# Kernel optimization log

Hardware: AMD Instinct MI355X
Metric: run time of the kernel (lower is better)

Reference implementation:

```python
import jax, jax.numpy as jnp
import numpy as np

N_NODES = 100000


def gcn_conv(x, edge_index, W, b):
    """PyG GCNConv: add self-loops, symmetric deg^-1/2 normalization, linear."""
    n = x.shape[0]
    h = x @ W  # [N, out]
    loop = jnp.arange(n, dtype=edge_index.dtype)
    src = jnp.concatenate([edge_index[0], loop])
    dst = jnp.concatenate([edge_index[1], loop])
    deg = jax.ops.segment_sum(jnp.ones_like(dst, dtype=h.dtype), dst, num_segments=n)
    dinv = jnp.where(deg > 0, jax.lax.rsqrt(deg), 0.0)
    norm = dinv[src] * dinv[dst]  # [E+N]
    msg = h[src] * norm[:, None]  # gather + scale
    out = jax.ops.segment_sum(msg, dst, num_segments=n)  # scatter-add
    return out + b


def setup_inputs() -> dict:
    key = jax.random.key(0)
    k1, k2, k3, k4 = jax.random.split(key, 4)
    d_in, d_hid, d_out = 128, 128, 128  # output_dim // 2 = 128
    E = 1600000
    x = jax.random.normal(k1, (N_NODES, d_in), dtype=jnp.float32)
    edge_index = jax.random.randint(k2, (2, E), 0, N_NODES, dtype=jnp.int64)
    s1 = 1.0 / np.sqrt(d_in)
    s2 = 1.0 / np.sqrt(d_hid)
    W1 = jax.random.normal(k3, (d_in, d_hid), dtype=jnp.float32) * s1
    b1 = jnp.zeros((d_hid,), dtype=jnp.float32)
    W2 = jax.random.normal(k4, (d_hid, d_out), dtype=jnp.float32) * s2
    b2 = jnp.zeros((d_out,), dtype=jnp.float32)
    return {"x": x, "edge_index": edge_index, "W1": W1, "b1": b1, "W2": W2, "b2": b2}


def reference(x, edge_index, W1, b1, W2, b2):
    h = jax.nn.relu(gcn_conv(x, edge_index, W1, b1))
    # dropout(p=0.5) is identity in eval mode
    return gcn_conv(h, edge_index, W2, b2)
```

## Files before the change

kernel.cpp:

```cpp
#include <hip/hip_runtime.h>

#define D 128

typedef unsigned int uint;
typedef unsigned short ushort;
typedef __attribute__((ext_vector_type(8))) short bf16x8_t;
typedef __attribute__((ext_vector_type(4))) float f32x4_t;

__global__ void k_init(int* __restrict__ degi, int n) {
    int i = blockIdx.x * blockDim.x + threadIdx.x;
    if (i < n) degi[i] = 1;
}

__global__ void k_count_rank(const int* __restrict__ dst, int* __restrict__ degi,
                             int* __restrict__ rank, int E) {
    int e = blockIdx.x * blockDim.x + threadIdx.x;
    if (e < E) rank[e] = atomicAdd(&degi[dst[e]], 1);
}

__global__ void k_dinv(const int* __restrict__ degi, float* __restrict__ dinv, int n) {
    int i = blockIdx.x * blockDim.x + threadIdx.x;
    if (i < n) dinv[i] = rsqrtf((float)degi[i]);
}

#define SCAN_BS 256
#define SCAN_ITEMS 4
#define SCAN_CHUNK (SCAN_BS * SCAN_ITEMS)

__device__ inline int count_at(const int* degi, int i, int n) {
    return (i < n) ? (degi[i] - 1) : 0;
}

__global__ void k_scan_partial(const int* __restrict__ degi, int* __restrict__ blockSums,
                               int n, int total) {
    __shared__ int s[SCAN_BS];
    int t = threadIdx.x;
    int base = blockIdx.x * SCAN_CHUNK + t * SCAN_ITEMS;
    int sum = 0;
    for (int j = 0; j < SCAN_ITEMS; j++) {
        int idx = base + j;
        if (idx < total) sum += count_at(degi, idx, n);
    }
    s[t] = sum; __syncthreads();
    for (int off = 1; off < SCAN_BS; off <<= 1) {
        int v = (t >= off) ? s[t - off] : 0;
        __syncthreads();
        s[t] += v;
        __syncthreads();
    }
    if (t == SCAN_BS - 1) blockSums[blockIdx.x] = s[t];
}

__global__ void k_scan_sums(int* __restrict__ blockSums, int nb) {
    __shared__ int s[1024];
    int t = threadIdx.x;
    int mine = (t < nb) ? blockSums[t] : 0;
    s[t] = mine; __syncthreads();
    for (int off = 1; off < 1024; off <<= 1) {
        int v = (t >= off) ? s[t - off] : 0;
        __syncthreads();
        s[t] += v;
        __syncthreads();
    }
    if (t < nb) blockSums[t] = s[t] - mine;
}

__global__ void k_scan_write(const int* __restrict__ degi, const int* __restrict__ blockSums,
                             int* __restrict__ row_ptr, int n, int total) {
    __shared__ int s[SCAN_BS];
    int t = threadIdx.x;
    int base = blockIdx.x * SCAN_CHUNK + t * SCAN_ITEMS;
    int c[SCAN_ITEMS];
    int sum = 0;
    for (int j = 0; j < SCAN_ITEMS; j++) {
        int idx = base + j;
        c[j] = (idx < total) ? count_at(degi, idx, n) : 0;
        sum += c[j];
    }
    int mine = sum;
    s[t] = sum; __syncthreads();
    for (int off = 1; off < SCAN_BS; off <<= 1) {
        int v = (t >= off) ? s[t - off] : 0;
        __syncthreads();
        s[t] += v;
        __syncthreads();
    }
    int off0 = blockSums[blockIdx.x] + (s[t] - mine);
    for (int j = 0; j < SCAN_ITEMS; j++) {
        int idx = base + j;
        if (idx < total) row_ptr[idx] = off0;
        off0 += c[j];
    }
}

__global__ void k_fill(const int* __restrict__ src, const int* __restrict__ dst,
                       const int* __restrict__ row_ptr, const int* __restrict__ rank,
                       int* __restrict__ col, int E) {
    int e = blockIdx.x * blockDim.x + threadIdx.x;
    if (e < E) {
        int d = dst[e];
        col[row_ptr[d] + rank[e] - 1] = src[e];
    }
}

__device__ inline uint bf16rn(float f) {
    uint u = __float_as_uint(f);
    return (u + 0x7fffu + ((u >> 16) & 1u)) >> 16;
}

__device__ inline void accum_bf16x8(float* a, uint4 v) {
    a[0] += __uint_as_float(v.x << 16);
    a[1] += __uint_as_float(v.x & 0xffff0000u);
    a[2] += __uint_as_float(v.y << 16);
    a[3] += __uint_as_float(v.y & 0xffff0000u);
    a[4] += __uint_as_float(v.z << 16);
    a[5] += __uint_as_float(v.z & 0xffff0000u);
    a[6] += __uint_as_float(v.w << 16);
    a[7] += __uint_as_float(v.w & 0xffff0000u);
}

__global__ void k_prep_w(const float* __restrict__ W, ushort* __restrict__ Wh,
                         ushort* __restrict__ Wl) {
    int i = blockIdx.x * blockDim.x + threadIdx.x;
    int k = i >> 7, n = i & 127;
    float w = W[k * D + n];
    uint hb = bf16rn(w);
    float hf = __uint_as_float(hb << 16);
    uint lb = bf16rn(w - hf);
    Wh[n * D + k] = (ushort)hb;
    Wl[n * D + k] = (ushort)lb;
}

template <bool A_FP32>
__global__ __launch_bounds__(256, 2) void k_gemm_mfma(const void* __restrict__ A,
                                                      const ushort* __restrict__ Wth,
                                                      const ushort* __restrict__ Wtl,
                                                      const float* __restrict__ dinv,
                                                      ushort* __restrict__ Yb, int M) {
    constexpr int STR = 72;
    constexpr int TILE = 128 * STR;
    __shared__ ushort lds[A_FP32 ? 4 * TILE : 3 * TILE];
    ushort* Ah = lds;
    ushort* Wh = lds + TILE;
    ushort* Wl = lds + 2 * TILE;
    ushort* Al = A_FP32 ? (lds + 3 * TILE) : nullptr;

    int t = threadIdx.x;
    int lane = t & 63, wave = t >> 6;
    int quad = lane >> 4, l16 = lane & 15;
    int m_off = (wave & 1) * 64;
    int n_off = (wave >> 1) * 64;
    int block_row = blockIdx.x * 128;

    f32x4_t acc[4][4];
#pragma unroll
    for (int mt = 0; mt < 4; mt++)
#pragma unroll
        for (int nt = 0; nt < 4; nt++) acc[mt][nt] = (f32x4_t){0.f, 0.f, 0.f, 0.f};

    for (int kc = 0; kc < 128; kc += 64) {
        if (A_FP32) {
            const float* Af = (const float*)A;
#pragma unroll
            for (int it = 0; it < 8; it++) {
                int s = t + it * 256;
                int row = s >> 4, kl = (s & 15) * 4;
                int gr = block_row + row;
                float4 v = make_float4(0.f, 0.f, 0.f, 0.f);
                if (gr < M) v = *(const float4*)(Af + (size_t)gr * D + kc + kl);
                ushort4 h, l;
                uint hb, lb; float hf;
                hb = bf16rn(v.x); hf = __uint_as_float(hb << 16); lb = bf16rn(v.x - hf);
                h.x = (ushort)hb; l.x = (ushort)lb;
                hb = bf16rn(v.y); hf = __uint_as_float(hb << 16); lb = bf16rn(v.y - hf);
                h.y = (ushort)hb; l.y = (ushort)lb;
                hb = bf16rn(v.z); hf = __uint_as_float(hb << 16); lb = bf16rn(v.z - hf);
                h.z = (ushort)hb; l.z = (ushort)lb;
                hb = bf16rn(v.w); hf = __uint_as_float(hb << 16); lb = bf16rn(v.w - hf);
                h.w = (ushort)hb; l.w = (ushort)lb;
                *(ushort4*)&Ah[row * STR + kl] = h;
                *(ushort4*)&Al[row * STR + kl] = l;
            }
        } else {
            const ushort* Ab = (const ushort*)A;
#pragma unroll
            for (int it = 0; it < 4; it++) {
                int s = t + it * 256;
                int row = s >> 3, kl = (s & 7) * 8;
                int gr = block_row + row;
                uint4 v = make_uint4(0u, 0u, 0u, 0u);
                if (gr < M) v = *(const uint4*)(Ab + (size_t)gr * D + kc + kl);
                *(uint4*)&Ah[row * STR + kl] = v;
            }
        }
#pragma unroll
        for (int it = 0; it < 4; it++) {
            int s = t + it * 256;
            int nrow = s >> 3, kl = (s & 7) * 8;
            *(uint4*)&Wh[nrow * STR + kl] = *(const uint4*)(Wth + nrow * D + kc + kl);
            *(uint4*)&Wl[nrow * STR + kl] = *(const uint4*)(Wtl + nrow * D + kc + kl);
        }
        __syncthreads();

#pragma unroll
        for (int ks = 0; ks < 2; ks++) {
            int kf = ks * 32 + quad * 8;
            bf16x8_t ah[4], bh[4], bl[4];
#pragma unroll
            for (int mt = 0; mt < 4; mt++)
                ah[mt] = *(const bf16x8_t*)&Ah[(m_off + mt * 16 + l16) * STR + kf];
#pragma unroll
            for (int nt = 0; nt < 4; nt++) {
                bh[nt] = *(const bf16x8_t*)&Wh[(n_off + nt * 16 + l16) * STR + kf];
                bl[nt] = *(const bf16x8_t*)&Wl[(n_off + nt * 16 + l16) * STR + kf];
            }
            if (A_FP32) {
                bf16x8_t al[4];
#pragma unroll
                for (int mt = 0; mt < 4; mt++)
                    al[mt] = *(const bf16x8_t*)&Al[(m_off + mt * 16 + l16) * STR + kf];
#pragma unroll
                for (int mt = 0; mt < 4; mt++)
#pragma unroll
                    for (int nt = 0; nt < 4; nt++) {
                        acc[mt][nt] = __builtin_amdgcn_mfma_f32_16x16x32_bf16(ah[mt], bh[nt], acc[mt][nt], 0, 0, 0);
                        acc[mt][nt] = __builtin_amdgcn_mfma_f32_16x16x32_bf16(al[mt], bh[nt], acc[mt][nt], 0, 0, 0);
                        acc[mt][nt] = __builtin_amdgcn_mfma_f32_16x16x32_bf16(ah[mt], bl[nt], acc[mt][nt], 0, 0, 0);
                    }
            } else {
#pragma unroll
                for (int mt = 0; mt < 4; mt++)
#pragma unroll
                    for (int nt = 0; nt < 4; nt++) {
                        acc[mt][nt] = __builtin_amdgcn_mfma_f32_16x16x32_bf16(ah[mt], bh[nt], acc[mt][nt], 0, 0, 0);
                        acc[mt][nt] = __builtin_amdgcn_mfma_f32_16x16x32_bf16(ah[mt], bl[nt], acc[mt][nt], 0, 0, 0);
                    }
            }
        }
        __syncthreads();
    }

#pragma unroll
    for (int mt = 0; mt < 4; mt++) {
#pragma unroll
        for (int reg = 0; reg < 4; reg++) {
            int gr = block_row + m_off + mt * 16 + quad * 4 + reg;
            if (gr < M) {
                float di = dinv[gr];
#pragma unroll
                for (int nt = 0; nt < 4; nt++) {
                    int colg = n_off + nt * 16 + l16;
                    Yb[(size_t)gr * D + colg] = (ushort)bf16rn(di * acc[mt][nt][reg]);
                }
            }
        }
    }
}

__global__ __launch_bounds__(256) void k_agg(const ushort* __restrict__ Hb,
                                             const int* __restrict__ row_ptr,
                                             const int* __restrict__ col,
                                             const float* __restrict__ dinv,
                                             const float* __restrict__ bias,
                                             float* __restrict__ Yf, ushort* __restrict__ Yb,
                                             int n, int do_relu, int out_bf16) {
    int node = blockIdx.x * 4 + (threadIdx.x >> 6);
    int lane = threadIdx.x & 63;
    int chain = lane >> 4;
    int l16   = lane & 15;
    if (node >= n) return;

    int start = row_ptr[node];
    int end   = row_ptr[node + 1];

    float a0[8], a1[8];
#pragma unroll
    for (int k = 0; k < 8; k++) { a0[k] = 0.f; a1[k] = 0.f; }

    if (chain == 0) {
        uint4 v = ((const uint4*)(Hb + (size_t)node * D))[l16];
        accum_bf16x8(a0, v);
    }

    int e = start + chain;
    for (; e + 4 < end; e += 8) {
        int s0 = col[e];
        int s1 = col[e + 4];
        uint4 v0 = ((const uint4*)(Hb + (size_t)s0 * D))[l16];
        uint4 v1 = ((const uint4*)(Hb + (size_t)s1 * D))[l16];
        accum_bf16x8(a0, v0);
        accum_bf16x8(a1, v1);
    }
    if (e < end) {
        int s0 = col[e];
        uint4 v0 = ((const uint4*)(Hb + (size_t)s0 * D))[l16];
        accum_bf16x8(a0, v0);
    }

    float acc[8];
#pragma unroll
    for (int k = 0; k < 8; k++) {
        float v = a0[k] + a1[k];
        v += __shfl_xor(v, 16, 64);
        v += __shfl_xor(v, 32, 64);
        acc[k] = v;
    }

    if (chain == 0) {
        float di = dinv[node];
        const float4* bp = (const float4*)bias + l16 * 2;
        float4 b0 = bp[0], b1 = bp[1];
        float o[8];
        o[0] = fmaf(di, acc[0], b0.x); o[1] = fmaf(di, acc[1], b0.y);
        o[2] = fmaf(di, acc[2], b0.z); o[3] = fmaf(di, acc[3], b0.w);
        o[4] = fmaf(di, acc[4], b1.x); o[5] = fmaf(di, acc[5], b1.y);
        o[6] = fmaf(di, acc[6], b1.z); o[7] = fmaf(di, acc[7], b1.w);
        if (do_relu) {
#pragma unroll
            for (int k = 0; k < 8; k++) o[k] = fmaxf(o[k], 0.f);
        }
        if (out_bf16) {
            uint4 pk;
            pk.x = bf16rn(o[0]) | (bf16rn(o[1]) << 16);
            pk.y = bf16rn(o[2]) | (bf16rn(o[3]) << 16);
            pk.z = bf16rn(o[4]) | (bf16rn(o[5]) << 16);
            pk.w = bf16rn(o[6]) | (bf16rn(o[7]) << 16);
            ((uint4*)(Yb + (size_t)node * D))[l16] = pk;
        } else {
            float4* yp = (float4*)(Yf + (size_t)node * D) + l16 * 2;
            yp[0] = make_float4(o[0], o[1], o[2], o[3]);
            yp[1] = make_float4(o[4], o[5], o[6], o[7]);
        }
    }
}

extern "C" void kernel_launch(void* const* d_in, const int* in_sizes, int n_in,
                              void* d_out, int out_size, void* d_ws, size_t ws_size,
                              hipStream_t stream) {
    const float* x  = (const float*)d_in[0];
    const int*   ei = (const int*)d_in[1];
    const float* W1 = (const float*)d_in[2];
    const float* b1 = (const float*)d_in[3];
    const float* W2 = (const float*)d_in[4];
    const float* b2 = (const float*)d_in[5];
    float* out = (float*)d_out;

    int n = in_sizes[0] / D;
    int E = in_sizes[1] / 2;
    const int* src = ei;
    const int* dst = ei + E;

    char* p = (char*)d_ws;
    ushort* h_buf = (ushort*)p; p += (size_t)n * D * sizeof(ushort);
    ushort* y_buf = (ushort*)p; p += (size_t)n * D * sizeof(ushort);
    ushort* w1h   = (ushort*)p; p += (size_t)D * D * sizeof(ushort);
    ushort* w1l   = (ushort*)p; p += (size_t)D * D * sizeof(ushort);
    ushort* w2h   = (ushort*)p; p += (size_t)D * D * sizeof(ushort);
    ushort* w2l   = (ushort*)p; p += (size_t)D * D * sizeof(ushort);
    float* dinv   = (float*)p;  p += (size_t)n * sizeof(float);
    int*   degi   = (int*)p;    p += (size_t)n * sizeof(int);
    int*   row_ptr= (int*)p;    p += (size_t)(n + 1) * sizeof(int);
    int*   bsums  = (int*)p;    p += 1024 * sizeof(int);
    int*   rank   = (int*)p;    p += (size_t)E * sizeof(int);
    int*   col    = (int*)p;    p += (size_t)E * sizeof(int);

    int total = n + 1;
    int nb = (total + SCAN_CHUNK - 1) / SCAN_CHUNK;

    k_init<<<(n + 255) / 256, 256, 0, stream>>>(degi, n);
    k_count_rank<<<(E + 255) / 256, 256, 0, stream>>>(dst, degi, rank, E);
    k_dinv<<<(n + 255) / 256, 256, 0, stream>>>(degi, dinv, n);
    k_scan_partial<<<nb, SCAN_BS, 0, stream>>>(degi, bsums, n, total);
    k_scan_sums<<<1, 1024, 0, stream>>>(bsums, nb);
    k_scan_write<<<nb, SCAN_BS, 0, stream>>>(degi, bsums, row_ptr, n, total);
    k_fill<<<(E + 255) / 256, 256, 0, stream>>>(src, dst, row_ptr, rank, col, E);

    k_prep_w<<<(D * D) / 256, 256, 0, stream>>>(W1, w1h, w1l);
    k_prep_w<<<(D * D) / 256, 256, 0, stream>>>(W2, w2h, w2l);

    int gemm_grid = (n + 127) / 128;
    int agg_grid  = (n + 3) / 4;

    k_gemm_mfma<true><<<gemm_grid, 256, 0, stream>>>(x, w1h, w1l, dinv, h_buf, n);
    k_agg<<<agg_grid, 256, 0, stream>>>(h_buf, row_ptr, col, dinv, b1, nullptr, y_buf, n, 1, 1);
    k_gemm_mfma<false><<<gemm_grid, 256, 0, stream>>>(y_buf, w2h, w2l, dinv, h_buf, n);
    k_agg<<<agg_grid, 256, 0, stream>>>(h_buf, row_ptr, col, dinv, b2, out, nullptr, n, 0, 0);
}
```

Before: 389.0 us.

## Build CSR via two-level bucket partition with shared-memory atomics

Replaces the global-atomic degree count, rank array, three-pass scan and random fill with a bucketed counting sort. Edges are first partitioned into 128-node buckets using per-block shared-memory histograms and a scanned block×bucket table. Each bucket is then sorted locally in shared memory to produce row_ptr, col and dinv. This avoids global atomics on a contended degree array and scattered writes, at the cost of an extra intermediate sorted array, more kernels, and only 128 blocks for the histogram and scatter passes, which may underuse the GPU.

```diff
diff --git a/kernel.cpp b/kernel.cpp
--- a/kernel.cpp
+++ b/kernel.cpp
@@ -7,99 +7,110 @@
 typedef __attribute__((ext_vector_type(8))) short bf16x8_t;
 typedef __attribute__((ext_vector_type(4))) float f32x4_t;
 
-__global__ void k_init(int* __restrict__ degi, int n) {
-    int i = blockIdx.x * blockDim.x + threadIdx.x;
-    if (i < n) degi[i] = 1;
-}
-
-__global__ void k_count_rank(const int* __restrict__ dst, int* __restrict__ degi,
-                             int* __restrict__ rank, int E) {
-    int e = blockIdx.x * blockDim.x + threadIdx.x;
-    if (e < E) rank[e] = atomicAdd(&degi[dst[e]], 1);
-}
-
-__global__ void k_dinv(const int* __restrict__ degi, float* __restrict__ dinv, int n) {
-    int i = blockIdx.x * blockDim.x + threadIdx.x;
-    if (i < n) dinv[i] = rsqrtf((float)degi[i]);
-}
-
-#define SCAN_BS 256
-#define SCAN_ITEMS 4
-#define SCAN_CHUNK (SCAN_BS * SCAN_ITEMS)
-
-__device__ inline int count_at(const int* degi, int i, int n) {
-    return (i < n) ? (degi[i] - 1) : 0;
-}
-
-__global__ void k_scan_partial(const int* __restrict__ degi, int* __restrict__ blockSums,
-                               int n, int total) {
-    __shared__ int s[SCAN_BS];
-    int t = threadIdx.x;
-    int base = blockIdx.x * SCAN_CHUNK + t * SCAN_ITEMS;
-    int sum = 0;
-    for (int j = 0; j < SCAN_ITEMS; j++) {
-        int idx = base + j;
-        if (idx < total) sum += count_at(degi, idx, n);
-    }
-    s[t] = sum; __syncthreads();
-    for (int off = 1; off < SCAN_BS; off <<= 1) {
-        int v = (t >= off) ? s[t - off] : 0;
-        __syncthreads();
-        s[t] += v;
-        __syncthreads();
-    }
-    if (t == SCAN_BS - 1) blockSums[blockIdx.x] = s[t];
-}
-
-__global__ void k_scan_sums(int* __restrict__ blockSums, int nb) {
+#define NB 128
+#define BSH 7
+#define BMASK 127
+#define MAXBUCK 1024
+
+__global__ __launch_bounds__(256) void kp_hist(const int* __restrict__ dst,
+                                               int* __restrict__ table,
+                                               int E, int nbuck, int chunk) {
+    __shared__ int h[MAXBUCK];
+    int t = threadIdx.x, b = blockIdx.x;
+    for (int i = t; i < nbuck; i += 256) h[i] = 0;
+    __syncthreads();
+    int s = b * chunk, e = min(E, s + chunk);
+    for (int i = s + t; i < e; i += 256)
+        atomicAdd(&h[dst[i] >> BSH], 1);
+    __syncthreads();
+    for (int i = t; i < nbuck; i += 256)
+        table[i * NB + b] = h[i];
+}
+
+__global__ void kp_scan_table(int* __restrict__ table, int* __restrict__ btot) {
+    __shared__ int s[NB];
+    int t = threadIdx.x, b = blockIdx.x;
+    int v = table[b * NB + t];
+    s[t] = v; __syncthreads();
+    for (int off = 1; off < NB; off <<= 1) {
+        int x = (t >= off) ? s[t - off] : 0;
+        __syncthreads();
+        s[t] += x;
+        __syncthreads();
+    }
+    table[b * NB + t] = s[t] - v;
+    if (t == NB - 1) btot[b] = s[t];
+}
+
+__global__ void kp_scan_btot(const int* __restrict__ btot, int* __restrict__ bucketBase,
+                             int* __restrict__ row_ptr, int nbuck, int E, int n) {
     __shared__ int s[1024];
     int t = threadIdx.x;
-    int mine = (t < nb) ? blockSums[t] : 0;
-    s[t] = mine; __syncthreads();
+    int v = (t < nbuck) ? btot[t] : 0;
+    s[t] = v; __syncthreads();
     for (int off = 1; off < 1024; off <<= 1) {
-        int v = (t >= off) ? s[t - off] : 0;
-        __syncthreads();
-        s[t] += v;
-        __syncthreads();
-    }
-    if (t < nb) blockSums[t] = s[t] - mine;
-}
-
-__global__ void k_scan_write(const int* __restrict__ degi, const int* __restrict__ blockSums,
-                             int* __restrict__ row_ptr, int n, int total) {
-    __shared__ int s[SCAN_BS];
-    int t = threadIdx.x;
-    int base = blockIdx.x * SCAN_CHUNK + t * SCAN_ITEMS;
-    int c[SCAN_ITEMS];
-    int sum = 0;
-    for (int j = 0; j < SCAN_ITEMS; j++) {
-        int idx = base + j;
-        c[j] = (idx < total) ? count_at(degi, idx, n) : 0;
-        sum += c[j];
-    }
-    int mine = sum;
-    s[t] = sum; __syncthreads();
-    for (int off = 1; off < SCAN_BS; off <<= 1) {
-        int v = (t >= off) ? s[t - off] : 0;
-        __syncthreads();
-        s[t] += v;
-        __syncthreads();
-    }
-    int off0 = blockSums[blockIdx.x] + (s[t] - mine);
-    for (int j = 0; j < SCAN_ITEMS; j++) {
-        int idx = base + j;
-        if (idx < total) row_ptr[idx] = off0;
-        off0 += c[j];
-    }
-}
-
-__global__ void k_fill(const int* __restrict__ src, const int* __restrict__ dst,
-                       const int* __restrict__ row_ptr, const int* __restrict__ rank,
-                       int* __restrict__ col, int E) {
-    int e = blockIdx.x * blockDim.x + threadIdx.x;
-    if (e < E) {
-        int d = dst[e];
-        col[row_ptr[d] + rank[e] - 1] = src[e];
+        int x = (t >= off) ? s[t - off] : 0;
+        __syncthreads();
+        s[t] += x;
+        __syncthreads();
+    }
+    if (t < nbuck) bucketBase[t] = s[t] - v;
+    if (t == 0) { bucketBase[nbuck] = E; row_ptr[n] = E; }
+}
+
+__global__ __launch_bounds__(256) void kp_scatter(const int* __restrict__ src,
+                                                  const int* __restrict__ dst,
+                                                  const int* __restrict__ table,
+                                                  const int* __restrict__ bucketBase,
+                                                  uint* __restrict__ sorted,
+                                                  int E, int nbuck, int chunk) {
+    __shared__ int off[MAXBUCK];
+    int t = threadIdx.x, b = blockIdx.x;
+    for (int i = t; i < nbuck; i += 256)
+        off[i] = bucketBase[i] + table[i * NB + b];
+    __syncthreads();
+    int s = b * chunk, e = min(E, s + chunk);
+    for (int i = s + t; i < e; i += 256) {
+        int d = dst[i];
+        int bk = d >> BSH;
+        int slot = atomicAdd(&off[bk], 1);
+        sorted[slot] = ((uint)src[i] << BSH) | (uint)(d & BMASK);
+    }
+}
+
+__global__ __launch_bounds__(256) void kp_build(const uint* __restrict__ sorted,
+                                                const int* __restrict__ bucketBase,
+                                                int* __restrict__ row_ptr,
+                                                int* __restrict__ col,
+                                                float* __restrict__ dinv, int n) {
+    __shared__ int cnt[128], loc[128], cnt2[128];
+    int t = threadIdx.x, b = blockIdx.x;
+    int base = bucketBase[b], end = bucketBase[b + 1];
+    if (t < 128) { cnt[t] = 0; cnt2[t] = 0; }
+    __syncthreads();
+    for (int i = base + t; i < end; i += 256)
+        atomicAdd(&cnt[sorted[i] & BMASK], 1);
+    __syncthreads();
+    int v = (t < 128) ? cnt[t] : 0;
+    if (t < 128) loc[t] = v;
+    __syncthreads();
+    for (int off = 1; off < 128; off <<= 1) {
+        int x = (t >= off && t < 128) ? loc[t - off] : 0;
+        __syncthreads();
+        if (t < 128) loc[t] += x;
+        __syncthreads();
+    }
+    int node = (b << BSH) + t;
+    if (t < 128 && node < n) {
+        row_ptr[node] = base + loc[t] - v;
+        dinv[node] = rsqrtf((float)(v + 1));
+    }
+    __syncthreads();
+    for (int i = base + t; i < end; i += 256) {
+        uint p = sorted[i];
+        int low = p & BMASK;
+        int r = atomicAdd(&cnt2[low], 1);
+        col[base + (loc[low] - cnt[low]) + r] = (int)(p >> BSH);
     }
 }
 
@@ -358,22 +369,21 @@
     ushort* w2h   = (ushort*)p; p += (size_t)D * D * sizeof(ushort);
     ushort* w2l   = (ushort*)p; p += (size_t)D * D * sizeof(ushort);
     float* dinv   = (float*)p;  p += (size_t)n * sizeof(float);
-    int*   degi   = (int*)p;    p += (size_t)n * sizeof(int);
     int*   row_ptr= (int*)p;    p += (size_t)(n + 1) * sizeof(int);
-    int*   bsums  = (int*)p;    p += 1024 * sizeof(int);
-    int*   rank   = (int*)p;    p += (size_t)E * sizeof(int);
+    int*   table  = (int*)p;    p += (size_t)MAXBUCK * NB * sizeof(int);
+    int*   btot   = (int*)p;    p += (size_t)MAXBUCK * sizeof(int);
+    int*   bbase  = (int*)p;    p += (size_t)(MAXBUCK + 1) * sizeof(int);
+    uint*  sorted = (uint*)p;   p += (size_t)E * sizeof(uint);
     int*   col    = (int*)p;    p += (size_t)E * sizeof(int);
 
-    int total = n + 1;
-    int nb = (total + SCAN_CHUNK - 1) / SCAN_CHUNK;
-
-    k_init<<<(n + 255) / 256, 256, 0, stream>>>(degi, n);
-    k_count_rank<<<(E + 255) / 256, 256, 0, stream>>>(dst, degi, rank, E);
-    k_dinv<<<(n + 255) / 256, 256, 0, stream>>>(degi, dinv, n);
-    k_scan_partial<<<nb, SCAN_BS, 0, stream>>>(degi, bsums, n, total);
-    k_scan_sums<<<1, 1024, 0, stream>>>(bsums, nb);
-    k_scan_write<<<nb, SCAN_BS, 0, stream>>>(degi, bsums, row_ptr, n, total);
-    k_fill<<<(E + 255) / 256, 256, 0, stream>>>(src, dst, row_ptr, rank, col, E);
+    int nbuck = (n + BMASK) >> BSH;
+    int chunk = (E + NB - 1) / NB;
+
+    kp_hist<<<NB, 256, 0, stream>>>(dst, table, E, nbuck, chunk);
+    kp_scan_table<<<nbuck, NB, 0, stream>>>(table, btot);
+    kp_scan_btot<<<1, 1024, 0, stream>>>(btot, bbase, row_ptr, nbuck, E, n);
+    kp_scatter<<<NB, 256, 0, stream>>>(src, dst, table, bbase, sorted, E, nbuck, chunk);
+    kp_build<<<nbuck, 256, 0, stream>>>(sorted, bbase, row_ptr, col, dinv, n);
 
     k_prep_w<<<(D * D) / 256, 256, 0, stream>>>(W1, w1h, w1l);
     k_prep_w<<<(D * D) / 256, 256, 0, stream>>>(W2, w2h, w2l);
```

New measurement: 355.1 us. -8.7%, faster.
